# Kernel tuning notes

Hardware: AMD Instinct MI355X
Metric: run time of the kernel (lower is better)

Reference implementation:

```python
import jax, jax.numpy as jnp
import numpy as np

THRESHOLD = 0.1
EPS = 1e-05


def setup_inputs() -> dict:
    key = jax.random.key(0)
    kx, kl, k1, k2 = jax.random.split(key, 4)
    B, S, D = 8, 4096, 1024
    Dh = max(2, D // 2)
    x = jax.random.normal(kx, (B, S, D), dtype=jnp.float32)
    # trailing (right) padding with random valid lengths in [S//2, S]
    lengths = jax.random.randint(kl, (B,), S // 2, S + 1)
    pad = jnp.arange(S)[None, :] >= lengths[:, None]  # [B, S] bool, True = padded
    W1 = jax.random.normal(k1, (D, Dh), dtype=jnp.float32) * (1.0 / np.sqrt(D))
    b1 = jnp.zeros((Dh,), dtype=jnp.float32)
    W2 = jax.random.normal(k2, (Dh, 1), dtype=jnp.float32) * (1.0 / np.sqrt(Dh))
    b2 = jnp.zeros((1,), dtype=jnp.float32)
    return {"x": x, "pad": pad, "W1": W1, "b1": b1, "W2": W2, "b2": b2}


def reference(x, pad, W1, b1, W2, b2):
    B, S, D = x.shape
    pos = jnp.arange(S)
    # number of valid (non-pad) tokens per batch; pad is trailing
    length = S - jnp.sum(pad, axis=1)  # [B]

    # tiny gate MLP: Linear -> ReLU -> Linear, squashed to (0, 1)
    h = jax.nn.relu(jnp.einsum('bsd,dh->bsh', x, W1) + b1)
    y = jnp.einsum('bsh,ho->bso', h, W2) + b2          # [B, S, 1]
    y = (1.0 + jnp.tanh(10.0 * y)) * 0.5

    # zero out gate values at padded positions (torch loop: y[i, n:] = 0)
    valid = pos[None, :] < length[:, None]             # [B, S]
    y = jnp.where(valid[..., None], y, 0.0)

    # lift so at least one token passes the threshold
    adjust = jnp.clip(EPS + THRESHOLD - jnp.max(y, axis=1), 0.0)  # [B, 1]
    y = y + adjust[:, None, :]                         # broadcast over seq

    u = x * y                                          # gated features [B, S, D]
    ys = y[..., 0]                                     # [B, S]
    u_mask = (ys > THRESHOLD) & (~pad)                 # tokens kept
    new_len = jnp.sum(u_mask, axis=1)                  # [B]

    # compact kept tokens to the front of each row (stable sort: kept first,
    # original order preserved) -- the mask-scatter v[v_mask] = u[u_mask]
    order = jnp.argsort(~u_mask, axis=1, stable=True)  # [B, S]
    v = jnp.take_along_axis(u, order[..., None], axis=1)
    v_mask = pos[None, :] < new_len[:, None]           # [B, S]
    v = jnp.where(v_mask[..., None], v, 0.0)
    v_pad = ~v_mask
    return v, v_pad
```

## Files before the change

### kernel.cpp

```cpp
#include <hip/hip_runtime.h>
#include <math.h>

#define NB 8
#define NS 4096
#define ND 1024
#define NDH 512
#define NTOK (NB*NS)
#define THRESH 0.1f
#define EPSV 1e-5f

using short8   = __attribute__((ext_vector_type(8)))  short;
using floatx16 = __attribute__((ext_vector_type(16))) float;
using floatv4  = __attribute__((ext_vector_type(4)))  float;

__device__ __forceinline__ unsigned short f32_to_bf16_rne(float f) {
  union { float f; unsigned u; } v; v.f = f;
  unsigned r = v.u + 0x7fffu + ((v.u >> 16) & 1u);
  return (unsigned short)(r >> 16);
}
__device__ __forceinline__ float bf16_to_f32(unsigned short h) {
  union { unsigned u; float f; } v; v.u = ((unsigned)h) << 16;
  return v.f;
}

__global__ __launch_bounds__(256)
void k0_prep(const float* __restrict__ W1, unsigned short* __restrict__ Wf,
             float* __restrict__ ysq) {
  __shared__ float sw[16][513];
  const int t = threadIdx.x;
  const int k16 = blockIdx.x;
  ysq[k16 * 512 + t] = 0.f;
  ysq[k16 * 512 + 256 + t] = 0.f;
#pragma unroll
  for (int i = 0; i < 8; ++i) {
    int flat = i * 256 + t;
    int r = flat >> 7, c4 = (flat & 127) << 2;
    *(float4*)&sw[r][c4] = *(const float4*)(W1 + (size_t)(k16 * 16 + r) * NDH + c4);
  }
  __syncthreads();
#pragma unroll
  for (int q = 0; q < 4; ++q) {
    int ss = q * 256 + t;
    int n32 = ss >> 6, lane = ss & 63;
    int n = n32 * 32 + (lane & 31);
    int kb = (lane >> 5) * 8;
    unsigned hi2[4], lo2[4];
#pragma unroll
    for (int j = 0; j < 4; ++j) {
      float w0 = sw[kb + 2 * j][n], w1 = sw[kb + 2 * j + 1][n];
      unsigned short h0 = f32_to_bf16_rne(w0), h1 = f32_to_bf16_rne(w1);
      unsigned short l0 = f32_to_bf16_rne(w0 - bf16_to_f32(h0));
      unsigned short l1 = f32_to_bf16_rne(w1 - bf16_to_f32(h1));
      hi2[j] = (unsigned)h0 | ((unsigned)h1 << 16);
      lo2[j] = (unsigned)l0 | ((unsigned)l1 << 16);
    }
    size_t cb = ((size_t)(n32 * 64 + k16) * 2) * 512 + (size_t)lane * 8;
    *(uint4*)(Wf + cb)       = make_uint4(hi2[0], hi2[1], hi2[2], hi2[3]);
    *(uint4*)(Wf + cb + 512) = make_uint4(lo2[0], lo2[1], lo2[2], lo2[3]);
  }
}

__global__ __launch_bounds__(256, 4)
void k1_gemm(const float* __restrict__ x, const unsigned short* __restrict__ Wf,
             const float* __restrict__ b1, const float* __restrict__ W2,
             float* __restrict__ ysq) {
  __shared__ __align__(16) unsigned short sx[2][2][64 * 72];
  __shared__ float red[4][64];

  const int tid = threadIdx.x;
  const int wave = tid >> 6, lane = tid & 63;
  const int l31 = lane & 31, h5 = lane >> 5;
  const int tok0 = (blockIdx.x >> 1) * 64;
  const int nhalf = blockIdx.x & 1;

  floatx16 acc[2][2];
#pragma unroll
  for (int mt = 0; mt < 2; ++mt)
#pragma unroll
    for (int nt = 0; nt < 2; ++nt)
#pragma unroll
      for (int r = 0; r < 16; ++r) acc[mt][nt][r] = 0.f;

  const int sm = tid >> 2;
  const int sk = (tid & 3) * 16;
  const float* xrow = x + (size_t)(tok0 + sm) * ND + sk;

  const unsigned short* wb[2];
#pragma unroll
  for (int nt = 0; nt < 2; ++nt) {
    const int n32 = nhalf * 8 + wave * 2 + nt;
    wb[nt] = Wf + (((size_t)n32 * 64) * 2) * 512 + (size_t)lane * 8;
  }

  auto stage_cvt = [&](int bf, const float4& a0, const float4& a1,
                       const float4& a2, const float4& a3) {
    float v16[16] = {a0.x, a0.y, a0.z, a0.w, a1.x, a1.y, a1.z, a1.w,
                     a2.x, a2.y, a2.z, a2.w, a3.x, a3.y, a3.z, a3.w};
    unsigned hp[8], lp[8];
#pragma unroll
    for (int j = 0; j < 8; ++j) {
      unsigned short h0 = f32_to_bf16_rne(v16[2 * j]);
      unsigned short h1 = f32_to_bf16_rne(v16[2 * j + 1]);
      unsigned short l0 = f32_to_bf16_rne(v16[2 * j] - bf16_to_f32(h0));
      unsigned short l1 = f32_to_bf16_rne(v16[2 * j + 1] - bf16_to_f32(h1));
      hp[j] = (unsigned)h0 | ((unsigned)h1 << 16);
      lp[j] = (unsigned)l0 | ((unsigned)l1 << 16);
    }
    *(uint4*)&sx[bf][0][sm * 72 + sk]     = make_uint4(hp[0], hp[1], hp[2], hp[3]);
    *(uint4*)&sx[bf][0][sm * 72 + sk + 8] = make_uint4(hp[4], hp[5], hp[6], hp[7]);
    *(uint4*)&sx[bf][1][sm * 72 + sk]     = make_uint4(lp[0], lp[1], lp[2], lp[3]);
    *(uint4*)&sx[bf][1][sm * 72 + sk + 8] = make_uint4(lp[4], lp[5], lp[6], lp[7]);
  };

  {
    float4 a0 = *(const float4*)xrow;
    float4 a1 = *(const float4*)(xrow + 4);
    float4 a2 = *(const float4*)(xrow + 8);
    float4 a3 = *(const float4*)(xrow + 12);
    stage_cvt(0, a0, a1, a2, a3);
  }

  for (int it = 0; it < 16; ++it) {
    const int p = it & 1;
    __syncthreads();
    float4 pa0, pa1, pa2, pa3;
    if (it < 15) {
      const float* xp = xrow + (it + 1) * 64;
      pa0 = *(const float4*)xp;
      pa1 = *(const float4*)(xp + 4);
      pa2 = *(const float4*)(xp + 8);
      pa3 = *(const float4*)(xp + 12);
    }
#pragma unroll
    for (int kh = 0; kh < 4; ++kh) {
      short8 bh[2], bl[2];
#pragma unroll
      for (int nt = 0; nt < 2; ++nt) {
        const unsigned short* q = wb[nt] + ((size_t)(4 * it + kh) * 2) * 512;
        bh[nt] = *(const short8*)(q);
        bl[nt] = *(const short8*)(q + 512);
      }
      short8 ah[2], al[2];
#pragma unroll
      for (int mt = 0; mt < 2; ++mt) {
        ah[mt] = *(const short8*)&sx[p][0][(mt * 32 + l31) * 72 + kh * 16 + h5 * 8];
        al[mt] = *(const short8*)&sx[p][1][(mt * 32 + l31) * 72 + kh * 16 + h5 * 8];
      }
#pragma unroll
      for (int nt = 0; nt < 2; ++nt)
#pragma unroll
        for (int mt = 0; mt < 2; ++mt)
          acc[mt][nt] = __builtin_amdgcn_mfma_f32_32x32x16_bf16(ah[mt], bh[nt], acc[mt][nt], 0, 0, 0);
#pragma unroll
      for (int nt = 0; nt < 2; ++nt)
#pragma unroll
        for (int mt = 0; mt < 2; ++mt)
          acc[mt][nt] = __builtin_amdgcn_mfma_f32_32x32x16_bf16(al[mt], bh[nt], acc[mt][nt], 0, 0, 0);
#pragma unroll
      for (int nt = 0; nt < 2; ++nt)
#pragma unroll
        for (int mt = 0; mt < 2; ++mt)
          acc[mt][nt] = __builtin_amdgcn_mfma_f32_32x32x16_bf16(ah[mt], bl[nt], acc[mt][nt], 0, 0, 0);
    }
    if (it < 15) stage_cvt(p ^ 1, pa0, pa1, pa2, pa3);
  }

  float b1v[2], w2v[2];
#pragma unroll
  for (int nt = 0; nt < 2; ++nt) {
    const int n = nhalf * 256 + wave * 64 + nt * 32 + l31;
    b1v[nt] = b1[n];
    w2v[nt] = W2[n];
  }
#pragma unroll
  for (int mt = 0; mt < 2; ++mt) {
    float pr[16];
#pragma unroll
    for (int r = 0; r < 16; ++r) pr[r] = 0.f;
#pragma unroll
    for (int nt = 0; nt < 2; ++nt)
#pragma unroll
      for (int r = 0; r < 16; ++r)
        pr[r] += fmaxf(acc[mt][nt][r] + b1v[nt], 0.f) * w2v[nt];
#pragma unroll
    for (int m = 1; m <= 16; m <<= 1)
#pragma unroll
      for (int r = 0; r < 16; ++r) pr[r] += __shfl_xor(pr[r], m, 64);
    if (l31 == 0) {
#pragma unroll
      for (int r = 0; r < 16; ++r) {
        int row = (r & 3) + 8 * (r >> 2) + 4 * h5;
        red[wave][mt * 32 + row] = pr[r];
      }
    }
  }
  __syncthreads();
  if (tid < 64) {
    float s = red[0][tid] + red[1][tid] + red[2][tid] + red[3][tid];
    atomicAdd(ysq + tok0 + tid, s);
  }
}

__global__ __launch_bounds__(1024)
void k2b(const float* __restrict__ ysq, const int* __restrict__ pad,
         const float* __restrict__ b2, float* __restrict__ gval,
         int* __restrict__ src_of_dest, int* __restrict__ new_len,
         float* __restrict__ vpad_out) {
  __shared__ int ssum[16];
  __shared__ float ssmax[16];
  const int b = blockIdx.x, tid = threadIdx.x;
  const int lane = tid & 63, wv = tid >> 6;
  const int base = b * NS, s0 = tid * 4;
  const float b2v = b2[0];

  float4 yq = *(const float4*)(ysq + base + s0);
  int4 pq = *(const int4*)(pad + base + s0);
  float yv[4] = {yq.x, yq.y, yq.z, yq.w};
  int pv[4] = {pq.x, pq.y, pq.z, pq.w};
  float m4 = 0.f;
#pragma unroll
  for (int i = 0; i < 4; ++i) {
    float y = (1.f + tanhf(10.f * (yv[i] + b2v))) * 0.5f;
    if (pv[i]) y = 0.f;
    yv[i] = y;
    m4 = fmaxf(m4, y);
  }
#pragma unroll
  for (int o = 32; o >= 1; o >>= 1) m4 = fmaxf(m4, __shfl_xor(m4, o, 64));
  if (lane == 0) ssmax[wv] = m4;
  __syncthreads();
  float rmax = ssmax[0];
#pragma unroll
  for (int w = 1; w < 16; ++w) rmax = fmaxf(rmax, ssmax[w]);
  const float adj = fmaxf(EPSV + THRESH - rmax, 0.f);

  unsigned km = 0;
  int cnt = 0;
#pragma unroll
  for (int i = 0; i < 4; ++i) {
    yv[i] += adj;
    bool keep = (yv[i] > THRESH) && !pv[i];
    if (keep) { km |= (1u << i); ++cnt; }
  }
  int inc = cnt;
#pragma unroll
  for (int o = 1; o < 64; o <<= 1) {
    int tmp = __shfl_up(inc, o, 64);
    if (lane >= o) inc += tmp;
  }
  if (lane == 63) ssum[wv] = inc;
  __syncthreads();
  int wpre = 0;
  int total = 0;
#pragma unroll
  for (int w = 0; w < 16; ++w) {
    int sv = ssum[w];
    if (w < wv) wpre += sv;
    total += sv;
  }
  int off = wpre + inc - cnt;
#pragma unroll
  for (int i = 0; i < 4; ++i) {
    int s = s0 + i;
    if ((km >> i) & 1u) {
      src_of_dest[base + off] = s;
      gval[base + off] = yv[i];
      ++off;
    }
    vpad_out[base + s] = (s >= total) ? 1.f : 0.f;
  }
  if (tid == 0) new_len[b] = total;
}

__global__ __launch_bounds__(256)
void k3_gather(const float* __restrict__ x, const float* __restrict__ gval,
               const int* __restrict__ src_of_dest, const int* __restrict__ new_len,
               float* __restrict__ v) {
  const int slot0 = blockIdx.x * 16;
  const int b = slot0 >> 12;
  const int nl = new_len[b];
  const int tid = threadIdx.x;
#pragma unroll
  for (int i = 0; i < 16; ++i) {
    const int slot = slot0 + i;
    const int dest = slot & (NS - 1);
    floatv4* vo = (floatv4*)(v + (size_t)slot * ND);
    floatv4 r;
    if (dest < nl) {
      const int src = src_of_dest[slot];
      const float g = gval[slot];
      floatv4 xv = ((const floatv4*)(x + ((size_t)b * NS + src) * ND))[tid];
      r = xv * g;
    } else {
      r = (floatv4)(0.f);
    }
    __builtin_nontemporal_store(r, vo + tid);
  }
}

extern "C" void kernel_launch(void* const* d_in, const int* in_sizes, int n_in,
                              void* d_out, int out_size, void* d_ws, size_t ws_size,
                              hipStream_t stream) {
  const float* x   = (const float*)d_in[0];
  const int*   pad = (const int*)d_in[1];
  const float* W1  = (const float*)d_in[2];
  const float* b1  = (const float*)d_in[3];
  const float* W2  = (const float*)d_in[4];
  const float* b2  = (const float*)d_in[5];

  float* v    = (float*)d_out;
  float* vpad = v + (size_t)NTOK * ND;

  unsigned short* Wf = (unsigned short*)(v + 24000000);

  float* ysq  = (float*)d_ws;
  float* gval = ysq + NTOK;
  int* src    = (int*)(gval + NTOK);
  int* nlen   = src + NTOK;

  k0_prep<<<64, 256, 0, stream>>>(W1, Wf, ysq);
  k1_gemm<<<NTOK / 32, 256, 0, stream>>>(x, Wf, b1, W2, ysq);
  k2b<<<NB, 1024, 0, stream>>>(ysq, pad, b2, gval, src, nlen, vpad);
  k3_gather<<<NTOK / 16, 256, 0, stream>>>(x, gval, src, nlen, v);
}
```

Before: 320.8 us.

## Software-pipeline B fragment loads and interleave x staging with MFMA phases

Double-buffers the weight fragments in registers so the next k-step's B loads are issued before the current MFMAs. The prefetch of the next x tile and its bf16 conversion into LDS are spread across the kh sub-steps. Explicit s_barrier/sched_barrier pairs and s_setprio around the MFMA block enforce a ping-pong schedule between waves. Occupancy is lowered in launch bounds to free registers for the extra buffers, at the cost of fewer resident waves and added barriers per sub-step.

```diff
diff --git a/kernel.cpp b/kernel.cpp
--- a/kernel.cpp
+++ b/kernel.cpp
@@ -60,7 +60,7 @@
   }
 }
 
-__global__ __launch_bounds__(256, 4)
+__global__ __launch_bounds__(256, 2)
 void k1_gemm(const float* __restrict__ x, const unsigned short* __restrict__ Wf,
              const float* __restrict__ b1, const float* __restrict__ W2,
              float* __restrict__ ysq) {
@@ -112,6 +112,16 @@
     *(uint4*)&sx[bf][1][sm * 72 + sk + 8] = make_uint4(lp[4], lp[5], lp[6], lp[7]);
   };
 
+  short8 Bh[2][2], Bl[2][2];
+  auto ldB = [&](int bf, int koff) {
+#pragma unroll
+    for (int nt = 0; nt < 2; ++nt) {
+      const unsigned short* q = wb[nt] + ((size_t)koff * 2) * 512;
+      Bh[bf][nt] = *(const short8*)(q);
+      Bl[bf][nt] = *(const short8*)(q + 512);
+    }
+  };
+
   {
     float4 a0 = *(const float4*)xrow;
     float4 a1 = *(const float4*)(xrow + 4);
@@ -119,50 +129,63 @@
     float4 a3 = *(const float4*)(xrow + 12);
     stage_cvt(0, a0, a1, a2, a3);
   }
-
+  ldB(0, 0);
+  asm volatile("s_waitcnt lgkmcnt(0)" ::: "memory");
+  __builtin_amdgcn_sched_barrier(0);
+  __builtin_amdgcn_s_barrier();
+  __builtin_amdgcn_sched_barrier(0);
+
+  float4 pa0, pa1, pa2, pa3;
   for (int it = 0; it < 16; ++it) {
     const int p = it & 1;
-    __syncthreads();
-    float4 pa0, pa1, pa2, pa3;
-    if (it < 15) {
-      const float* xp = xrow + (it + 1) * 64;
-      pa0 = *(const float4*)xp;
-      pa1 = *(const float4*)(xp + 4);
-      pa2 = *(const float4*)(xp + 8);
-      pa3 = *(const float4*)(xp + 12);
-    }
 #pragma unroll
     for (int kh = 0; kh < 4; ++kh) {
-      short8 bh[2], bl[2];
-#pragma unroll
-      for (int nt = 0; nt < 2; ++nt) {
-        const unsigned short* q = wb[nt] + ((size_t)(4 * it + kh) * 2) * 512;
-        bh[nt] = *(const short8*)(q);
-        bl[nt] = *(const short8*)(q + 512);
-      }
+      const int cur = kh & 1, nxt = cur ^ 1;
       short8 ah[2], al[2];
 #pragma unroll
       for (int mt = 0; mt < 2; ++mt) {
         ah[mt] = *(const short8*)&sx[p][0][(mt * 32 + l31) * 72 + kh * 16 + h5 * 8];
         al[mt] = *(const short8*)&sx[p][1][(mt * 32 + l31) * 72 + kh * 16 + h5 * 8];
       }
+      if (!(it == 15 && kh == 3))
+        ldB(nxt, 4 * it + kh + 1);
+      if (kh == 0 && it < 15) {
+        const float* xp = xrow + (it + 1) * 64;
+        pa0 = *(const float4*)xp;
+        pa1 = *(const float4*)(xp + 4);
+        pa2 = *(const float4*)(xp + 8);
+        pa3 = *(const float4*)(xp + 12);
+      }
+      if (kh == 2 && it < 15)
+        stage_cvt(p ^ 1, pa0, pa1, pa2, pa3);
+      if (kh == 3) {
+        asm volatile("s_waitcnt lgkmcnt(0)" ::: "memory");
+        __builtin_amdgcn_sched_barrier(0);
+      }
+      __builtin_amdgcn_sched_barrier(0);
+      __builtin_amdgcn_s_barrier();
+      __builtin_amdgcn_sched_barrier(0);
+      __builtin_amdgcn_s_setprio(1);
 #pragma unroll
       for (int nt = 0; nt < 2; ++nt)
 #pragma unroll
         for (int mt = 0; mt < 2; ++mt)
-          acc[mt][nt] = __builtin_amdgcn_mfma_f32_32x32x16_bf16(ah[mt], bh[nt], acc[mt][nt], 0, 0, 0);
+          acc[mt][nt] = __builtin_amdgcn_mfma_f32_32x32x16_bf16(ah[mt], Bh[cur][nt], acc[mt][nt], 0, 0, 0);
 #pragma unroll
       for (int nt = 0; nt < 2; ++nt)
 #pragma unroll
         for (int mt = 0; mt < 2; ++mt)
-          acc[mt][nt] = __builtin_amdgcn_mfma_f32_32x32x16_bf16(al[mt], bh[nt], acc[mt][nt], 0, 0, 0);
+          acc[mt][nt] = __builtin_amdgcn_mfma_f32_32x32x16_bf16(al[mt], Bh[cur][nt], acc[mt][nt], 0, 0, 0);
 #pragma unroll
       for (int nt = 0; nt < 2; ++nt)
 #pragma unroll
         for (int mt = 0; mt < 2; ++mt)
-          acc[mt][nt] = __builtin_amdgcn_mfma_f32_32x32x16_bf16(ah[mt], bl[nt], acc[mt][nt], 0, 0, 0);
-    }
-    if (it < 15) stage_cvt(p ^ 1, pa0, pa1, pa2, pa3);
+          acc[mt][nt] = __builtin_amdgcn_mfma_f32_32x32x16_bf16(ah[mt], Bl[cur][nt], acc[mt][nt], 0, 0, 0);
+      __builtin_amdgcn_s_setprio(0);
+      __builtin_amdgcn_sched_barrier(0);
+      __builtin_amdgcn_s_barrier();
+      __builtin_amdgcn_sched_barrier(0);
+    }
   }
 
   float b1v[2], w2v[2];
```

Result: no change. 322.2 us (+0.4%).
